# Optimization experiments

Hardware: AMD Instinct MI355X
Metric: run time of the kernel (lower is better)

The kernel has to match this reference:

```python
import jax, jax.numpy as jnp
import numpy as np

TEMPERATURE = 0.5
EPS = 1e-8  # torch CosineSimilarity default eps


def setup_inputs() -> dict:
    key = jax.random.key(0)
    k1, k2 = jax.random.split(key)
    N, D = 4096, 256
    return {
        "batch_embeddings": jax.random.normal(k1, (N, D), dtype=jnp.float32),
        "batch_augmented_embeddings": jax.random.normal(k2, (N, D), dtype=jnp.float32),
    }


def reference(batch_embeddings, batch_augmented_embeddings):
    N = batch_embeddings.shape[0]
    emb = jnp.concatenate([batch_embeddings, batch_augmented_embeddings], axis=0)  # (2N, D)
    # cosine similarity = normalized dot products (normalize + GEMM rewrite of the
    # broadcasted nn.CosineSimilarity)
    norms = jnp.sqrt(jnp.sum(emb * emb, axis=-1, keepdims=True))
    emb_n = emb / jnp.maximum(norms, EPS)
    sim = jnp.einsum("id,jd->ij", emb_n, emb_n) / TEMPERATURE  # (2N, 2N)
    # negative mask: (~eye(N)).repeat(2,2) -> False where (i mod N) == (j mod N)
    idx = jnp.arange(2 * N)
    neg_mask = (idx[:, None] % N) != (idx[None, :] % N)
    exp_sim = jnp.exp(sim) * neg_mask.astype(sim.dtype)
    sum_exp = jnp.sum(exp_sim, axis=-1)  # (2N,)
    pos = jnp.arange(N)
    positive_sim = sim[pos, N + pos]  # (N,)
    negative_sim_sum = sum_exp[:N]  # (N,)
    loss = -jnp.mean(jnp.log(jnp.exp(positive_sim) / negative_sim_sum))
    return loss
```

## Files before the change

### kernel.cpp

```cpp
#include <hip/hip_runtime.h>
#include <hip/hip_bf16.h>

#define NROWS 4096
#define DDIM  256
#define EPS   1e-8f
#define SCALE 1.69864944f
#define LN2   0.69314718056f

#define NJ 32
#define JS 256
#define BT 64
#define CH (JS / BT)
#define BUFSH (4 * 8 * 64 * 8)

typedef __attribute__((ext_vector_type(8))) short short8;
typedef __attribute__((ext_vector_type(4))) float f32x4;

#if __has_builtin(__builtin_amdgcn_exp2f)
#define EXP2F(x) __builtin_amdgcn_exp2f(x)
#else
#define EXP2F(x) exp2f(x)
#endif

#define CFENCE() asm volatile("" ::: "memory")
#define BARRIER() do { CFENCE(); __builtin_amdgcn_s_barrier(); CFENCE(); } while (0)

__device__ __forceinline__ unsigned short f2bf(float x) {
    union { __hip_bfloat16 h; unsigned short u; } c;
    c.h = __float2bfloat16(x);
    return c.u;
}

__device__ __forceinline__ float bf2f(unsigned short u) {
    union { float f; unsigned int i; } c;
    c.i = ((unsigned int)u) << 16;
    return c.f;
}

__global__ void normalize_kernel(const float* __restrict__ a,
                                 const float* __restrict__ b,
                                 unsigned short* __restrict__ en,
                                 float* __restrict__ S, int N) {
    const int wave = threadIdx.x >> 6, lane = threadIdx.x & 63;
    const int row = blockIdx.x * 4 + wave;
    const float* src = (row < N) ? (a + (size_t)row * DDIM)
                                 : (b + (size_t)(row - N) * DDIM);
    const float4 v = reinterpret_cast<const float4*>(src)[lane];
    float ss = v.x * v.x + v.y * v.y + v.z * v.z + v.w * v.w;
    #pragma unroll
    for (int off = 32; off > 0; off >>= 1) ss += __shfl_xor(ss, off);
    const float inv = SCALE / fmaxf(sqrtf(ss), EPS * SCALE);
    ushort4 o;
    o.x = f2bf(v.x * inv);
    o.y = f2bf(v.y * inv);
    o.z = f2bf(v.z * inv);
    o.w = f2bf(v.w * inv);
    *reinterpret_cast<ushort4*>(en + (size_t)row * DDIM + lane * 4) = o;
    if (lane == 0 && row < N) S[row] = 0.0f;
}

__global__ void pos_kernel(const unsigned short* __restrict__ en,
                           float* __restrict__ pos, int N) {
    const int wave = threadIdx.x >> 6, lane = threadIdx.x & 63;
    const int row = blockIdx.x * 4 + wave;
    const ushort4 u = *reinterpret_cast<const ushort4*>(
        en + (size_t)row * DDIM + lane * 4);
    const ushort4 w = *reinterpret_cast<const ushort4*>(
        en + (size_t)(N + row) * DDIM + lane * 4);
    float d = bf2f(u.x) * bf2f(w.x) + bf2f(u.y) * bf2f(w.y) +
              bf2f(u.z) * bf2f(w.z) + bf2f(u.w) * bf2f(w.w);
    #pragma unroll
    for (int off = 32; off > 0; off >>= 1) d += __shfl_xor(d, off);
    if (lane == 0) pos[row] = d * LN2;
}

__global__ __launch_bounds__(256, 2) void simsum_kernel(
        const short* __restrict__ en,
        float* __restrict__ S) {
    __shared__ short bt[2 * BUFSH];
    const int tid = threadIdx.x;
    const int wave = tid >> 6, lane = tid & 63;
    const int lrow = lane & 15, quad = lane >> 4;
    const int i0 = blockIdx.x * 256 + wave * 64;
    const int jb = blockIdx.y * JS;

    short8 afrag[4][8];
    #pragma unroll
    for (int t = 0; t < 4; ++t)
        #pragma unroll
        for (int ks = 0; ks < 8; ++ks)
            afrag[t][ks] = *reinterpret_cast<const short8*>(
                en + (size_t)(i0 + t * 16 + lrow) * DDIM + ks * 32 + quad * 8);

    float rowsum[4][4];
    #pragma unroll
    for (int t = 0; t < 4; ++t)
        #pragma unroll
        for (int r = 0; r < 4; ++r) rowsum[t][r] = 0.0f;

    auto stage = [&](int jc, int buf) {
        const short* g = en + (size_t)(jc + wave * 16 + lrow) * DDIM + quad * 8;
        short* l = bt + buf * BUFSH + wave * 4096;
        #pragma unroll
        for (int ks = 0; ks < 8; ++ks) {
            __builtin_amdgcn_global_load_lds(
                (const __attribute__((address_space(1))) void*)(g + ks * 32),
                (__attribute__((address_space(3))) void*)(l + ks * 512),
                16, 0, 0);
        }
    };

    stage(jb, 0);
    for (int c = 0; c < CH; ++c) {
        asm volatile("s_waitcnt lgkmcnt(0)" ::: "memory");
        BARRIER();
        if (c + 1 < CH) {
            stage(jb + (c + 1) * BT, (c + 1) & 1);
            asm volatile("s_waitcnt vmcnt(8)" ::: "memory");
        } else {
            asm volatile("s_waitcnt vmcnt(0)" ::: "memory");
        }
        __builtin_amdgcn_sched_barrier(0);
        BARRIER();
        const short* lb = bt + (c & 1) * BUFSH;
        #pragma unroll
        for (int cg = 0; cg < 4; ++cg) {
            f32x4 acc[4];
            #pragma unroll
            for (int t = 0; t < 4; ++t) acc[t] = f32x4{0.f, 0.f, 0.f, 0.f};
            __builtin_amdgcn_s_setprio(1);
            #pragma unroll
            for (int ks = 0; ks < 8; ++ks) {
                const short8 bfrag = *reinterpret_cast<const short8*>(
                    lb + cg * 4096 + ks * 512 + lane * 8);
                #pragma unroll
                for (int t = 0; t < 4; ++t)
                    acc[t] = __builtin_amdgcn_mfma_f32_16x16x32_bf16(
                        afrag[t][ks], bfrag, acc[t], 0, 0, 0);
            }
            __builtin_amdgcn_s_setprio(0);
            const int cm = (jb + c * BT + cg * 16 + lrow) & (NROWS - 1);
            #pragma unroll
            for (int t = 0; t < 4; ++t) {
                const int dd = cm - (i0 + t * 16 + quad * 4);
                #pragma unroll
                for (int r = 0; r < 4; ++r) {
                    const float ed = EXP2F(acc[t][r]);
                    rowsum[t][r] += (dd == r) ? 0.0f : ed;
                }
            }
        }
    }

    #pragma unroll
    for (int t = 0; t < 4; ++t) {
        #pragma unroll
        for (int r = 0; r < 4; ++r) {
            float v = rowsum[t][r];
            v += __shfl_xor(v, 1);
            v += __shfl_xor(v, 2);
            v += __shfl_xor(v, 4);
            v += __shfl_xor(v, 8);
            rowsum[t][r] = v;
        }
        if (lrow < 4) {
            const float v = (lrow == 0) ? rowsum[t][0]
                          : (lrow == 1) ? rowsum[t][1]
                          : (lrow == 2) ? rowsum[t][2]
                          :               rowsum[t][3];
            atomicAdd(&S[i0 + t * 16 + quad * 4 + lrow], v);
        }
    }
}

__global__ void loss_kernel(const float* __restrict__ S,
                            const float* __restrict__ pos,
                            float* __restrict__ out, int N) {
    const int i = threadIdx.x * 4;
    float acc = 0.0f;
    if (i < N) {
        const float4 s4 = *reinterpret_cast<const float4*>(S + i);
        const float4 p4 = *reinterpret_cast<const float4*>(pos + i);
        acc = (p4.x - __logf(s4.x)) + (p4.y - __logf(s4.y)) +
              (p4.z - __logf(s4.z)) + (p4.w - __logf(s4.w));
    }
    #pragma unroll
    for (int off = 32; off > 0; off >>= 1) acc += __shfl_xor(acc, off);
    __shared__ float wsum[16];
    const int wave = threadIdx.x >> 6, lane = threadIdx.x & 63;
    if (lane == 0) wsum[wave] = acc;
    __syncthreads();
    if (threadIdx.x == 0) {
        float tot = 0.0f;
        #pragma unroll
        for (int w = 0; w < 16; ++w) tot += wsum[w];
        out[0] = -tot / (float)N;
    }
}

extern "C" void kernel_launch(void* const* d_in, const int* in_sizes, int n_in,
                              void* d_out, int out_size, void* d_ws, size_t ws_size,
                              hipStream_t stream) {
    const float* a = (const float*)d_in[0];
    const float* b = (const float*)d_in[1];
    float* out = (float*)d_out;
    const int N = NROWS;

    char* ws = (char*)d_ws;
    unsigned short* en = (unsigned short*)ws;
    float* S = (float*)(ws + (size_t)2 * N * DDIM * sizeof(unsigned short));
    float* pos = S + N;

    normalize_kernel<<<(2 * N) / 4, 256, 0, stream>>>(a, b, en, S, N);
    pos_kernel<<<N / 4, 256, 0, stream>>>(en, pos, N);
    simsum_kernel<<<dim3(N / 256, NJ), 256, 0, stream>>>((const short*)en, S);
    loss_kernel<<<1, 1024, 0, stream>>>(S, pos, out, N);
}
```

Baseline: 89.34 us.

## Fuse normalize with positive dot and fold loss into last GEMM block

Normalization of both views and the positive-pair dot product now run in one prep kernel, which computes the dot from the bf16 values it just produced instead of reloading them. The final loss reduction moves into the similarity kernel: each block bumps a global counter and the last block to finish reads S through atomics and writes the loss. This cuts four launches to two and removes one pass over the normalized embeddings. The cost is a threadfence and counter atomic per block, plus a serial tail where a single block reduces 4096 values.

After: 117.4 us. 1.31x slower.

```diff
diff --git a/kernel.cpp b/kernel.cpp
--- a/kernel.cpp
+++ b/kernel.cpp
@@ -37,47 +37,52 @@
     return c.f;
 }
 
-__global__ void normalize_kernel(const float* __restrict__ a,
-                                 const float* __restrict__ b,
-                                 unsigned short* __restrict__ en,
-                                 float* __restrict__ S, int N) {
+__global__ void prep_kernel(const float* __restrict__ a,
+                            const float* __restrict__ b,
+                            unsigned short* __restrict__ en,
+                            float* __restrict__ S,
+                            float* __restrict__ pos,
+                            unsigned int* __restrict__ counter, int N) {
     const int wave = threadIdx.x >> 6, lane = threadIdx.x & 63;
     const int row = blockIdx.x * 4 + wave;
-    const float* src = (row < N) ? (a + (size_t)row * DDIM)
-                                 : (b + (size_t)(row - N) * DDIM);
-    const float4 v = reinterpret_cast<const float4*>(src)[lane];
-    float ss = v.x * v.x + v.y * v.y + v.z * v.z + v.w * v.w;
-    #pragma unroll
-    for (int off = 32; off > 0; off >>= 1) ss += __shfl_xor(ss, off);
-    const float inv = SCALE / fmaxf(sqrtf(ss), EPS * SCALE);
-    ushort4 o;
-    o.x = f2bf(v.x * inv);
-    o.y = f2bf(v.y * inv);
-    o.z = f2bf(v.z * inv);
-    o.w = f2bf(v.w * inv);
-    *reinterpret_cast<ushort4*>(en + (size_t)row * DDIM + lane * 4) = o;
-    if (lane == 0 && row < N) S[row] = 0.0f;
-}
-
-__global__ void pos_kernel(const unsigned short* __restrict__ en,
-                           float* __restrict__ pos, int N) {
-    const int wave = threadIdx.x >> 6, lane = threadIdx.x & 63;
-    const int row = blockIdx.x * 4 + wave;
-    const ushort4 u = *reinterpret_cast<const ushort4*>(
-        en + (size_t)row * DDIM + lane * 4);
-    const ushort4 w = *reinterpret_cast<const ushort4*>(
-        en + (size_t)(N + row) * DDIM + lane * 4);
-    float d = bf2f(u.x) * bf2f(w.x) + bf2f(u.y) * bf2f(w.y) +
-              bf2f(u.z) * bf2f(w.z) + bf2f(u.w) * bf2f(w.w);
+    const float4 va = reinterpret_cast<const float4*>(a + (size_t)row * DDIM)[lane];
+    const float4 vb = reinterpret_cast<const float4*>(b + (size_t)row * DDIM)[lane];
+    float ssa = va.x * va.x + va.y * va.y + va.z * va.z + va.w * va.w;
+    float ssb = vb.x * vb.x + vb.y * vb.y + vb.z * vb.z + vb.w * vb.w;
+    #pragma unroll
+    for (int off = 32; off > 0; off >>= 1) {
+        ssa += __shfl_xor(ssa, off);
+        ssb += __shfl_xor(ssb, off);
+    }
+    const float inva = SCALE / fmaxf(sqrtf(ssa), EPS * SCALE);
+    const float invb = SCALE / fmaxf(sqrtf(ssb), EPS * SCALE);
+    ushort4 oa, ob;
+    oa.x = f2bf(va.x * inva); oa.y = f2bf(va.y * inva);
+    oa.z = f2bf(va.z * inva); oa.w = f2bf(va.w * inva);
+    ob.x = f2bf(vb.x * invb); ob.y = f2bf(vb.y * invb);
+    ob.z = f2bf(vb.z * invb); ob.w = f2bf(vb.w * invb);
+    *reinterpret_cast<ushort4*>(en + (size_t)row * DDIM + lane * 4) = oa;
+    *reinterpret_cast<ushort4*>(en + (size_t)(N + row) * DDIM + lane * 4) = ob;
+    float d = bf2f(oa.x) * bf2f(ob.x) + bf2f(oa.y) * bf2f(ob.y) +
+              bf2f(oa.z) * bf2f(ob.z) + bf2f(oa.w) * bf2f(ob.w);
     #pragma unroll
     for (int off = 32; off > 0; off >>= 1) d += __shfl_xor(d, off);
-    if (lane == 0) pos[row] = d * LN2;
+    if (lane == 0) {
+        pos[row] = d * LN2;
+        S[row] = 0.0f;
+        if (row == 0) counter[0] = 0u;
+    }
 }
 
 __global__ __launch_bounds__(256, 2) void simsum_kernel(
         const short* __restrict__ en,
-        float* __restrict__ S) {
+        float* __restrict__ S,
+        const float* __restrict__ pos,
+        unsigned int* __restrict__ counter,
+        float* __restrict__ out) {
     __shared__ short bt[2 * BUFSH];
+    __shared__ unsigned int lastflag;
+    __shared__ float wsum[4];
     const int tid = threadIdx.x;
     const int wave = tid >> 6, lane = tid & 63;
     const int lrow = lane & 15, quad = lane >> 4;
@@ -171,30 +176,23 @@
             atomicAdd(&S[i0 + t * 16 + quad * 4 + lrow], v);
         }
     }
-}
-
-__global__ void loss_kernel(const float* __restrict__ S,
-                            const float* __restrict__ pos,
-                            float* __restrict__ out, int N) {
-    const int i = threadIdx.x * 4;
-    float acc = 0.0f;
-    if (i < N) {
-        const float4 s4 = *reinterpret_cast<const float4*>(S + i);
-        const float4 p4 = *reinterpret_cast<const float4*>(pos + i);
-        acc = (p4.x - __logf(s4.x)) + (p4.y - __logf(s4.y)) +
-              (p4.z - __logf(s4.z)) + (p4.w - __logf(s4.w));
-    }
-    #pragma unroll
-    for (int off = 32; off > 0; off >>= 1) acc += __shfl_xor(acc, off);
-    __shared__ float wsum[16];
-    const int wave = threadIdx.x >> 6, lane = threadIdx.x & 63;
-    if (lane == 0) wsum[wave] = acc;
+
+    __threadfence();
     __syncthreads();
-    if (threadIdx.x == 0) {
-        float tot = 0.0f;
-        #pragma unroll
-        for (int w = 0; w < 16; ++w) tot += wsum[w];
-        out[0] = -tot / (float)N;
+    if (tid == 0) lastflag = atomicAdd(counter, 1u);
+    __syncthreads();
+    if (lastflag == (unsigned)(gridDim.x * gridDim.y) - 1u) {
+        float acc = 0.0f;
+        for (int i = tid; i < NROWS; i += 256) {
+            const float sv = atomicAdd(&S[i], 0.0f);
+            acc += pos[i] - __logf(sv);
+        }
+        #pragma unroll
+        for (int off = 32; off > 0; off >>= 1) acc += __shfl_xor(acc, off);
+        if (lane == 0) wsum[wave] = acc;
+        __syncthreads();
+        if (tid == 0)
+            out[0] = -(wsum[0] + wsum[1] + wsum[2] + wsum[3]) / (float)NROWS;
     }
 }
 
@@ -210,9 +208,9 @@
     unsigned short* en = (unsigned short*)ws;
     float* S = (float*)(ws + (size_t)2 * N * DDIM * sizeof(unsigned short));
     float* pos = S + N;
-
-    normalize_kernel<<<(2 * N) / 4, 256, 0, stream>>>(a, b, en, S, N);
-    pos_kernel<<<N / 4, 256, 0, stream>>>(en, pos, N);
-    simsum_kernel<<<dim3(N / 256, NJ), 256, 0, stream>>>((const short*)en, S);
-    loss_kernel<<<1, 1024, 0, stream>>>(S, pos, out, N);
-}
+    unsigned int* counter = (unsigned int*)(pos + N);
+
+    prep_kernel<<<N / 4, 256, 0, stream>>>(a, b, en, S, pos, counter, N);
+    simsum_kernel<<<dim3(N / 256, NJ), 256, 0, stream>>>((const short*)en, S,
+                                                         pos, counter, out);
+}
```
